# Performance work log

Hardware: AMD Instinct MI355X
Metric: run time of the kernel (lower is better)

## Reference

```python
import jax, jax.numpy as jnp
import numpy as np

E = 8          # num_experts
TOP_K = 2      # num_experts_per_tok
H = 1024       # hidden_size
F = 2048       # intermediate_size
B, S = 2, 4096


def setup_inputs() -> dict:
    key = jax.random.key(0)
    ks = jax.random.split(key, 5)
    hidden_states = jax.random.normal(ks[0], (B, S, H), dtype=jnp.float32)
    gate_w = jax.random.normal(ks[1], (E, H), dtype=jnp.float32) * 0.02   # router: logits = x @ gate_w.T
    Wg = jax.random.normal(ks[2], (E, H, F), dtype=jnp.float32) * 0.02    # gate_proj per expert
    Wu = jax.random.normal(ks[3], (E, H, F), dtype=jnp.float32) * 0.02    # up_proj per expert
    Wd = jax.random.normal(ks[4], (E, F, H), dtype=jnp.float32) * 0.02    # down_proj per expert
    return {"hidden_states": hidden_states, "gate_w": gate_w, "Wg": Wg, "Wu": Wu, "Wd": Wd}


def reference(hidden_states, gate_w, Wg, Wu, Wd):
    b, s, h = hidden_states.shape
    x = hidden_states.reshape(-1, h)                       # [T, H]
    T = x.shape[0]

    router_logits = x @ gate_w.T                           # [T, E]
    probs = jax.nn.softmax(router_logits.astype(jnp.float32), axis=-1)
    topk_w, topk_idx = jax.lax.top_k(probs, TOP_K)         # [T, K]
    topk_w = topk_w / jnp.sum(topk_w, axis=-1, keepdims=True)  # norm_topk_prob
    topk_w = topk_w.astype(x.dtype)

    # Dense per-token-per-expert combine weight (0 for unselected experts).
    w_full = jnp.zeros((T, E), dtype=x.dtype)
    w_full = w_full.at[jnp.arange(T)[:, None], topk_idx].add(topk_w)  # [T, E]

    out = jnp.zeros_like(x)
    for e in range(E):  # fixed small loop over experts
        g = jax.nn.silu(x @ Wg[e]) * (x @ Wu[e])           # [T, F]
        out = out + w_full[:, e:e + 1] * (g @ Wd[e])       # [T, H]

    return out.reshape(b, s, h), router_logits
```

## Files before the change

### kernel.cpp

```cpp
#include <hip/hip_runtime.h>
#include <cstdint>

#define NTOK   8192
#define HDIM   1024
#define FDIM   2048
#define NEXP   8
#define RTOT   (2*NTOK)
#define RPAD   128

typedef unsigned short u16;
typedef short   bf16x8 __attribute__((ext_vector_type(8)));
typedef float   f32x4  __attribute__((ext_vector_type(4)));
typedef u16     u16x8  __attribute__((ext_vector_type(8)));

__device__ __forceinline__ u16 f2bf(float v) {
  union { float f; uint32_t u; } a; a.f = v;
  uint32_t r = a.u + 0x7FFFu + ((a.u >> 16) & 1u);
  return (u16)(r >> 16);
}
__device__ __forceinline__ float bf2f(u16 b) {
  union { uint32_t u; float f; } a; a.u = ((uint32_t)b) << 16; return a.f;
}

__global__ void router_kernel(const float* __restrict__ x, const float* __restrict__ gw,
                              float* __restrict__ logits, int* __restrict__ te,
                              float* __restrict__ tw) {
  int gid  = blockIdx.x * blockDim.x + threadIdx.x;
  int t    = gid >> 6;
  int lane = gid & 63;
  const float4* xr = (const float4*)(x + (size_t)t * HDIM);
  float acc[NEXP];
#pragma unroll
  for (int e = 0; e < NEXP; ++e) acc[e] = 0.f;
#pragma unroll
  for (int c = 0; c < 4; ++c) {
    float4 xv = xr[c * 64 + lane];
#pragma unroll
    for (int e = 0; e < NEXP; ++e) {
      float4 wv = ((const float4*)(gw + e * HDIM))[c * 64 + lane];
      acc[e] += xv.x * wv.x + xv.y * wv.y + xv.z * wv.z + xv.w * wv.w;
    }
  }
#pragma unroll
  for (int off = 32; off > 0; off >>= 1)
#pragma unroll
    for (int e = 0; e < NEXP; ++e) acc[e] += __shfl_xor(acc[e], off, 64);

  if (lane == 0) {
#pragma unroll
    for (int e = 0; e < NEXP; ++e) logits[(size_t)t * NEXP + e] = acc[e];
    int e1 = 0;
#pragma unroll
    for (int e = 1; e < NEXP; ++e) if (acc[e] > acc[e1]) e1 = e;
    int e2 = -1;
#pragma unroll
    for (int e = 0; e < NEXP; ++e) {
      if (e == e1) continue;
      if (e2 < 0 || acc[e] > acc[e2]) e2 = e;
    }
    float m  = fmaxf(acc[e1], acc[e2]);
    float p1 = __expf(acc[e1] - m), p2 = __expf(acc[e2] - m);
    float inv = 1.f / (p1 + p2);
    te[t * 2]     = e1;  tw[t * 2]     = p1 * inv;
    te[t * 2 + 1] = e2;  tw[t * 2 + 1] = p2 * inv;
  }
}

__global__ void count_prefix_kernel(const int* __restrict__ te, int* __restrict__ offs,
                                    int* __restrict__ cursors) {
  __shared__ int wsum[16][NEXP];
  int cnt[NEXP];
#pragma unroll
  for (int e = 0; e < NEXP; ++e) cnt[e] = 0;
  for (int i = threadIdx.x; i < 2 * NTOK; i += 1024) {
    int v = te[i];
#pragma unroll
    for (int e = 0; e < NEXP; ++e) cnt[e] += (v == e) ? 1 : 0;
  }
#pragma unroll
  for (int off = 32; off > 0; off >>= 1)
#pragma unroll
    for (int e = 0; e < NEXP; ++e) cnt[e] += __shfl_xor(cnt[e], off, 64);
  int wave = threadIdx.x >> 6, lane = threadIdx.x & 63;
  if (lane == 0)
#pragma unroll
    for (int e = 0; e < NEXP; ++e) wsum[wave][e] = cnt[e];
  __syncthreads();
  if (threadIdx.x == 0) {
    int s = 0;
    for (int e = 0; e < NEXP; ++e) {
      int c = 0;
      for (int w = 0; w < 16; ++w) c += wsum[w][e];
      offs[e] = s; cursors[e * 16] = s; s += c;
    }
    offs[NEXP] = s;
  }
}

__global__ void scatter_kernel(const int* __restrict__ te, const float* __restrict__ tw,
                               int* __restrict__ cursors, int* __restrict__ tok_ids,
                               float* __restrict__ wts, int* __restrict__ slots) {
  int t    = blockIdx.x * blockDim.x + threadIdx.x;
  int lane = threadIdx.x & 63;
#pragma unroll
  for (int s = 0; s < 2; ++s) {
    int   e = te[t * 2 + s];
    float w = tw[t * 2 + s];
    int pos = 0;
#pragma unroll
    for (int e0 = 0; e0 < NEXP; ++e0) {
      unsigned long long m = __ballot(e == e0);
      if (e == e0) {
        int leader = __ffsll((unsigned long long)m) - 1;
        int rank   = __popcll(m & ((1ull << lane) - 1ull));
        int b = 0;
        if (lane == leader) b = atomicAdd(&cursors[e0 * 16], (int)__popcll(m));
        b = __shfl(b, leader, 64);
        pos = b + rank;
      }
    }
    tok_ids[pos] = t;
    wts[pos] = w;
    slots[t * 2 + s] = pos;
  }
}

__global__ void gather_cast_kernel(const float* __restrict__ x, const int* __restrict__ tok_ids,
                                   u16* __restrict__ Xg) {
  int j = blockIdx.x;
  int t = tok_ids[j];
  float4 v = ((const float4*)(x + (size_t)t * HDIM))[threadIdx.x];
  ushort4 o;
  o.x = f2bf(v.x); o.y = f2bf(v.y); o.z = f2bf(v.z); o.w = f2bf(v.w);
  ((ushort4*)(Xg + (size_t)j * HDIM))[threadIdx.x] = o;
}

__global__ __launch_bounds__(256)
void prep_weights_kernel(const float* __restrict__ Wg, const float* __restrict__ Wu,
                         const float* __restrict__ Wd, u16* __restrict__ Wgt,
                         u16* __restrict__ Wut, u16* __restrict__ Wdt) {
  __shared__ float tile[64 * 65];
  const int mat = blockIdx.z >> 3;
  const int e   = blockIdx.z & 7;
  const int K   = (mat < 2) ? HDIM : FDIM;
  const int N   = (mat < 2) ? FDIM : HDIM;
  const float* src = ((mat == 0) ? Wg : (mat == 1) ? Wu : Wd) + (size_t)e * K * N;
  u16*         dst = ((mat == 0) ? Wgt : (mat == 1) ? Wut : Wdt) + (size_t)e * K * N;
  const int tn = (mat < 2) ? blockIdx.x : blockIdx.y;
  const int tk = (mat < 2) ? blockIdx.y : blockIdx.x;
  const int k0 = tk * 64, n0 = tn * 64;

  const int r  = threadIdx.x >> 2;
  const int c4 = threadIdx.x & 3;
#pragma unroll
  for (int i = 0; i < 4; ++i) {
    int c = (c4 + i * 4) * 4;
    float4 v = *(const float4*)(src + (size_t)(k0 + r) * N + n0 + c);
    tile[r * 65 + c]     = v.x;
    tile[r * 65 + c + 1] = v.y;
    tile[r * 65 + c + 2] = v.z;
    tile[r * 65 + c + 3] = v.w;
  }
  __syncthreads();

  const int kq = threadIdx.x & 7;
  const int nr = threadIdx.x >> 3;
#pragma unroll
  for (int p = 0; p < 2; ++p) {
    int n = p * 32 + nr;
    u16x8 pk;
#pragma unroll
    for (int j = 0; j < 8; ++j)
      pk[j] = f2bf(tile[(kq * 8 + j) * 65 + n]);
    *(u16x8*)(dst + (size_t)(n0 + n) * K + k0 + kq * 8) = pk;
  }
}

__device__ __forceinline__ void stage_tile(const u16* __restrict__ src, int ld,
                                           u16* __restrict__ lds, int wave, int lane) {
#pragma unroll
  for (int i = 0; i < 4; ++i) {
    int chunk = ((i << 2) + wave) << 9;
    int flat  = chunk + (lane << 3);
    int row   = flat >> 6;
    int km    = (flat & 63) ^ ((row & 7) << 3);
    __builtin_amdgcn_global_load_lds(
        (const __attribute__((address_space(1))) uint32_t*)(src + (size_t)row * ld + km),
        (__attribute__((address_space(3))) uint32_t*)(lds + chunk),
        16, 0, 0);
  }
}

__global__ __launch_bounds__(256, 2)
void gemm1_kernel(const u16* __restrict__ Xg, const u16* __restrict__ Wgt,
                  const u16* __restrict__ Wut, const int* __restrict__ offs,
                  u16* __restrict__ G) {
  const int e     = blockIdx.z;
  const int rbase = offs[e];
  const int rows  = offs[e + 1] - rbase;
  const int row0  = blockIdx.y * 128;
  if (row0 >= rows) return;
  const int n0    = blockIdx.x * 128;
  const int arow0 = rbase + row0;

  __shared__ __align__(16) u16 As[128 * 64];
  __shared__ __align__(16) u16 Bgs[128 * 64];
  __shared__ __align__(16) u16 Bus[128 * 64];

  const int tid  = threadIdx.x;
  const int wave = tid >> 6;
  const int lane = tid & 63;
  const int wm   = wave >> 1, wn = wave & 1;
  const int l15  = lane & 15, quad = lane >> 4;

  const u16* Ag = Xg  + (size_t)arow0 * HDIM;
  const u16* Bg = Wgt + (size_t)e * FDIM * HDIM + (size_t)n0 * HDIM;
  const u16* Bu = Wut + (size_t)e * FDIM * HDIM + (size_t)n0 * HDIM;

  f32x4 accg[4][4], accu[4][4];
#pragma unroll
  for (int i = 0; i < 4; ++i)
#pragma unroll
    for (int j = 0; j < 4; ++j) { accg[i][j] = (f32x4)0.f; accu[i][j] = (f32x4)0.f; }

  for (int kt = 0; kt < HDIM / 64; ++kt) {
    const int k0 = kt * 64;
    stage_tile(Ag + k0, HDIM, As,  wave, lane);
    stage_tile(Bg + k0, HDIM, Bgs, wave, lane);
    stage_tile(Bu + k0, HDIM, Bus, wave, lane);
    __syncthreads();
#pragma unroll
    for (int kk = 0; kk < 64; kk += 32) {
      bf16x8 af[4];
#pragma unroll
      for (int im = 0; im < 4; ++im) {
        int r  = wm * 64 + im * 16 + l15;
        int kq = (kk + quad * 8) ^ ((r & 7) << 3);
        af[im] = *(const bf16x8*)(As + r * 64 + kq);
      }
#pragma unroll
      for (int in = 0; in < 4; ++in) {
        int r  = wn * 64 + in * 16 + l15;
        int kq = (kk + quad * 8) ^ ((r & 7) << 3);
        bf16x8 bg = *(const bf16x8*)(Bgs + r * 64 + kq);
        bf16x8 bu = *(const bf16x8*)(Bus + r * 64 + kq);
#pragma unroll
        for (int im = 0; im < 4; ++im) {
          accg[im][in] = __builtin_amdgcn_mfma_f32_16x16x32_bf16(af[im], bg, accg[im][in], 0, 0, 0);
          accu[im][in] = __builtin_amdgcn_mfma_f32_16x16x32_bf16(af[im], bu, accu[im][in], 0, 0, 0);
        }
      }
    }
    __syncthreads();
  }

#pragma unroll
  for (int im = 0; im < 4; ++im) {
#pragma unroll
    for (int rr = 0; rr < 4; ++rr) {
      int lrow = row0 + wm * 64 + im * 16 + quad * 4 + rr;
      if (lrow < rows) {
        size_t grow = (size_t)(rbase + lrow);
#pragma unroll
        for (int in = 0; in < 4; ++in) {
          float g = accg[im][in][rr];
          float u = accu[im][in][rr];
          float val = g / (1.f + __expf(-g)) * u;
          int gcol = n0 + wn * 64 + in * 16 + l15;
          G[grow * FDIM + gcol] = f2bf(val);
        }
      }
    }
  }
}

__global__ __launch_bounds__(256, 2)
void gemm2_kernel(const u16* __restrict__ G, const u16* __restrict__ Wdt,
                  const int* __restrict__ offs, const float* __restrict__ wts,
                  u16* __restrict__ Y) {
  const int e     = blockIdx.z;
  const int rbase = offs[e];
  const int rows  = offs[e + 1] - rbase;
  const int row0  = blockIdx.y * 128;
  if (row0 >= rows) return;
  const int n0    = blockIdx.x * 128;
  const int arow0 = rbase + row0;

  __shared__ __align__(16) u16 As[128 * 64];
  __shared__ __align__(16) u16 Bs[128 * 64];

  const int tid  = threadIdx.x;
  const int wave = tid >> 6;
  const int lane = tid & 63;
  const int wm   = wave >> 1, wn = wave & 1;
  const int l15  = lane & 15, quad = lane >> 4;

  const u16* Ag = G   + (size_t)arow0 * FDIM;
  const u16* Bg = Wdt + (size_t)e * HDIM * FDIM + (size_t)n0 * FDIM;

  f32x4 acc[4][4];
#pragma unroll
  for (int i = 0; i < 4; ++i)
#pragma unroll
    for (int j = 0; j < 4; ++j) acc[i][j] = (f32x4)0.f;

  for (int kt = 0; kt < FDIM / 64; ++kt) {
    const int k0 = kt * 64;
    stage_tile(Ag + k0, FDIM, As, wave, lane);
    stage_tile(Bg + k0, FDIM, Bs, wave, lane);
    __syncthreads();
#pragma unroll
    for (int kk = 0; kk < 64; kk += 32) {
      bf16x8 af[4], bf[4];
#pragma unroll
      for (int im = 0; im < 4; ++im) {
        int r  = wm * 64 + im * 16 + l15;
        int kq = (kk + quad * 8) ^ ((r & 7) << 3);
        af[im] = *(const bf16x8*)(As + r * 64 + kq);
      }
#pragma unroll
      for (int in = 0; in < 4; ++in) {
        int r  = wn * 64 + in * 16 + l15;
        int kq = (kk + quad * 8) ^ ((r & 7) << 3);
        bf[in] = *(const bf16x8*)(Bs + r * 64 + kq);
      }
#pragma unroll
      for (int in = 0; in < 4; ++in)
#pragma unroll
        for (int im = 0; im < 4; ++im)
          acc[im][in] = __builtin_amdgcn_mfma_f32_16x16x32_bf16(af[im], bf[in], acc[im][in], 0, 0, 0);
    }
    __syncthreads();
  }

#pragma unroll
  for (int im = 0; im < 4; ++im) {
#pragma unroll
    for (int rr = 0; rr < 4; ++rr) {
      int lrow = row0 + wm * 64 + im * 16 + quad * 4 + rr;
      if (lrow < rows) {
        int grow = rbase + lrow;
        float w  = wts[grow];
        u16* yrow = Y + (size_t)grow * HDIM + n0 + wn * 64 + l15;
#pragma unroll
        for (int in = 0; in < 4; ++in)
          yrow[in * 16] = f2bf(acc[im][in][rr] * w);
      }
    }
  }
}

__global__ void combine_kernel(const u16* __restrict__ Y, const int* __restrict__ slots,
                               float* __restrict__ out) {
  int t  = blockIdx.x;
  int s1 = slots[2 * t], s2 = slots[2 * t + 1];
  ushort4 a = ((const ushort4*)(Y + (size_t)s1 * HDIM))[threadIdx.x];
  ushort4 b = ((const ushort4*)(Y + (size_t)s2 * HDIM))[threadIdx.x];
  float4 o;
  o.x = bf2f(a.x) + bf2f(b.x);
  o.y = bf2f(a.y) + bf2f(b.y);
  o.z = bf2f(a.z) + bf2f(b.z);
  o.w = bf2f(a.w) + bf2f(b.w);
  ((float4*)(out + (size_t)t * HDIM))[threadIdx.x] = o;
}

extern "C" void kernel_launch(void* const* d_in, const int* in_sizes, int n_in,
                              void* d_out, int out_size, void* d_ws, size_t ws_size,
                              hipStream_t stream) {
  const float* x  = (const float*)d_in[0];
  const float* gw = (const float*)d_in[1];
  const float* Wg = (const float*)d_in[2];
  const float* Wu = (const float*)d_in[3];
  const float* Wd = (const float*)d_in[4];

  float* out    = (float*)d_out;
  float* logits = out + (size_t)NTOK * HDIM;

  char* p = (char*)d_ws;
  u16* Wgt = (u16*)p;  p += (size_t)NEXP * FDIM * HDIM * 2;
  u16* Wut = (u16*)p;  p += (size_t)NEXP * FDIM * HDIM * 2;
  u16* Wdt = (u16*)p;  p += (size_t)NEXP * HDIM * FDIM * 2;
  u16* Xg  = (u16*)p;  p += (size_t)(RTOT + RPAD) * HDIM * 2;
  u16* G   = (u16*)p;  p += (size_t)(RTOT + RPAD) * FDIM * 2;
  int*   tok_ids = (int*)p;   p += (RTOT + RPAD) * 4;
  float* wts     = (float*)p; p += (RTOT + RPAD) * 4;
  int*   te      = (int*)p;   p += NTOK * 2 * 4;
  float* tw      = (float*)p; p += NTOK * 2 * 4;
  int*   slots   = (int*)p;   p += NTOK * 2 * 4;
  int*   offs    = (int*)p;   p += (NEXP + 1) * 4;
  int*   cursors = (int*)p;   p += NEXP * 16 * 4;

  u16* Y = Xg;

  router_kernel<<<(NTOK * 64) / 256, 256, 0, stream>>>(x, gw, logits, te, tw);
  count_prefix_kernel<<<1, 1024, 0, stream>>>(te, offs, cursors);
  scatter_kernel<<<NTOK / 256, 256, 0, stream>>>(te, tw, cursors, tok_ids, wts, slots);
  gather_cast_kernel<<<RTOT, 256, 0, stream>>>(x, tok_ids, Xg);

  prep_weights_kernel<<<dim3(32, 16, 24), 256, 0, stream>>>(Wg, Wu, Wd, Wgt, Wut, Wdt);

  gemm1_kernel<<<dim3(FDIM / 128, 64, NEXP), 256, 0, stream>>>(Xg, Wgt, Wut, offs, G);
  gemm2_kernel<<<dim3(HDIM / 128, 64, NEXP), 256, 0, stream>>>(G, Wdt, offs, wts, Y);
  combine_kernel<<<NTOK, 256, 0, stream>>>(Y, slots, out);
}
```

Measured before the change: 554.9 us.

## Rewrite expert GEMMs as 256x128 tiles, 8 waves, double-buffered LDS pipeline

Both grouped GEMMs move from 128x128 tiles with 4 waves to 256x128 tiles with 8 waves. LDS is double-buffered, and the global-to-LDS loads for the next K-tile are interleaved with the MFMA phases. Explicit vmcnt waits, raw barriers, sched_barriers and setprio control the schedule. The aim is to hide load latency behind compute and raise operand reuse per block. In exchange, the larger LDS footprint (96KB for gemm1) may limit occupancy, the larger row tile wastes more work on padding, and the hand-placed waits and barriers are fragile.

```diff
diff --git a/kernel.cpp b/kernel.cpp
--- a/kernel.cpp
+++ b/kernel.cpp
@@ -6,7 +6,7 @@
 #define FDIM   2048
 #define NEXP   8
 #define RTOT   (2*NTOK)
-#define RPAD   128
+#define RPAD   256
 
 typedef unsigned short u16;
 typedef short   bf16x8 __attribute__((ext_vector_type(8)));
@@ -176,178 +176,273 @@
   }
 }
 
-__device__ __forceinline__ void stage_tile(const u16* __restrict__ src, int ld,
+
+#define BARRIER()  asm volatile("s_barrier" ::: "memory")
+#define SCHEDB()   __builtin_amdgcn_sched_barrier(0)
+#define WAITVM(n)  asm volatile("s_waitcnt vmcnt(" #n ")" ::: "memory")
+
+__device__ __forceinline__ void stage_half(const u16* __restrict__ src, int ld,
                                            u16* __restrict__ lds, int wave, int lane) {
 #pragma unroll
-  for (int i = 0; i < 4; ++i) {
-    int chunk = ((i << 2) + wave) << 9;
-    int flat  = chunk + (lane << 3);
-    int row   = flat >> 6;
-    int km    = (flat & 63) ^ ((row & 7) << 3);
+  for (int s = 0; s < 2; ++s) {
+    const int base = (s * 8 + wave) << 9;
+    const int flat = base + (lane << 3);
+    const int row  = flat >> 6;
+    const int km   = (flat & 63) ^ ((row & 7) << 3);
     __builtin_amdgcn_global_load_lds(
         (const __attribute__((address_space(1))) uint32_t*)(src + (size_t)row * ld + km),
-        (__attribute__((address_space(3))) uint32_t*)(lds + chunk),
+        (__attribute__((address_space(3))) uint32_t*)(lds + base),
         16, 0, 0);
   }
 }
 
-__global__ __launch_bounds__(256, 2)
+template<int MH>
+__device__ __forceinline__ void rd_a(const u16* __restrict__ buf, bf16x8 (&aH)[2][4],
+                                     int wm, int l15, int quad) {
+#pragma unroll
+  for (int k2 = 0; k2 < 2; ++k2)
+#pragma unroll
+    for (int im = 0; im < 4; ++im) {
+      const int r  = MH * 128 + wm * 64 + im * 16 + l15;
+      const int kq = (k2 * 32 + quad * 8) ^ ((r & 7) << 3);
+      aH[k2][im] = *(const bf16x8*)(buf + r * 64 + kq);
+    }
+}
+
+__device__ __forceinline__ void rd_b(const u16* __restrict__ buf, int rb, bf16x8 (&bb)[2][2],
+                                     int l15, int quad) {
+#pragma unroll
+  for (int k2 = 0; k2 < 2; ++k2)
+#pragma unroll
+    for (int in = 0; in < 2; ++in) {
+      const int r  = rb + in * 16 + l15;
+      const int kq = (k2 * 32 + quad * 8) ^ ((r & 7) << 3);
+      bb[k2][in] = *(const bf16x8*)(buf + r * 64 + kq);
+    }
+}
+
+__device__ __forceinline__ void mm16(const bf16x8 (&aH)[2][4], const bf16x8 (&bb)[2][2],
+                                     f32x4 (&ac)[4][2]) {
+#pragma unroll
+  for (int k2 = 0; k2 < 2; ++k2)
+#pragma unroll
+    for (int im = 0; im < 4; ++im)
+#pragma unroll
+      for (int in = 0; in < 2; ++in)
+        ac[im][in] = __builtin_amdgcn_mfma_f32_16x16x32_bf16(aH[k2][im], bb[k2][in],
+                                                             ac[im][in], 0, 0, 0);
+}
+
+__global__ __launch_bounds__(512, 2)
 void gemm1_kernel(const u16* __restrict__ Xg, const u16* __restrict__ Wgt,
                   const u16* __restrict__ Wut, const int* __restrict__ offs,
                   u16* __restrict__ G) {
   const int e     = blockIdx.z;
   const int rbase = offs[e];
   const int rows  = offs[e + 1] - rbase;
-  const int row0  = blockIdx.y * 128;
+  const int row0  = blockIdx.y * 256;
   if (row0 >= rows) return;
   const int n0    = blockIdx.x * 128;
-  const int arow0 = rbase + row0;
-
-  __shared__ __align__(16) u16 As[128 * 64];
-  __shared__ __align__(16) u16 Bgs[128 * 64];
-  __shared__ __align__(16) u16 Bus[128 * 64];
+
+  __shared__ __align__(16) u16 As [2][256 * 64];
+  __shared__ __align__(16) u16 Bgs[2][128 * 64];
+  __shared__ __align__(16) u16 Bus[2][128 * 64];
 
   const int tid  = threadIdx.x;
   const int wave = tid >> 6;
   const int lane = tid & 63;
-  const int wm   = wave >> 1, wn = wave & 1;
+  const int wm   = wave >> 2, wn = wave & 3;
   const int l15  = lane & 15, quad = lane >> 4;
 
-  const u16* Ag = Xg  + (size_t)arow0 * HDIM;
-  const u16* Bg = Wgt + (size_t)e * FDIM * HDIM + (size_t)n0 * HDIM;
-  const u16* Bu = Wut + (size_t)e * FDIM * HDIM + (size_t)n0 * HDIM;
-
-  f32x4 accg[4][4], accu[4][4];
-#pragma unroll
-  for (int i = 0; i < 4; ++i)
-#pragma unroll
-    for (int j = 0; j < 4; ++j) { accg[i][j] = (f32x4)0.f; accu[i][j] = (f32x4)0.f; }
-
-  for (int kt = 0; kt < HDIM / 64; ++kt) {
-    const int k0 = kt * 64;
-    stage_tile(Ag + k0, HDIM, As,  wave, lane);
-    stage_tile(Bg + k0, HDIM, Bgs, wave, lane);
-    stage_tile(Bu + k0, HDIM, Bus, wave, lane);
-    __syncthreads();
-#pragma unroll
-    for (int kk = 0; kk < 64; kk += 32) {
-      bf16x8 af[4];
-#pragma unroll
-      for (int im = 0; im < 4; ++im) {
-        int r  = wm * 64 + im * 16 + l15;
-        int kq = (kk + quad * 8) ^ ((r & 7) << 3);
-        af[im] = *(const bf16x8*)(As + r * 64 + kq);
-      }
-#pragma unroll
-      for (int in = 0; in < 4; ++in) {
-        int r  = wn * 64 + in * 16 + l15;
-        int kq = (kk + quad * 8) ^ ((r & 7) << 3);
-        bf16x8 bg = *(const bf16x8*)(Bgs + r * 64 + kq);
-        bf16x8 bu = *(const bf16x8*)(Bus + r * 64 + kq);
-#pragma unroll
-        for (int im = 0; im < 4; ++im) {
-          accg[im][in] = __builtin_amdgcn_mfma_f32_16x16x32_bf16(af[im], bg, accg[im][in], 0, 0, 0);
-          accu[im][in] = __builtin_amdgcn_mfma_f32_16x16x32_bf16(af[im], bu, accu[im][in], 0, 0, 0);
+  const u16* Ap  = Xg  + (size_t)(rbase + row0) * HDIM;
+  const u16* Bgp = Wgt + (size_t)e * FDIM * HDIM + (size_t)n0 * HDIM;
+  const u16* Bup = Wut + (size_t)e * FDIM * HDIM + (size_t)n0 * HDIM;
+
+  f32x4 accg[2][4][2], accu[2][4][2];
+#pragma unroll
+  for (int h = 0; h < 2; ++h)
+#pragma unroll
+    for (int i = 0; i < 4; ++i)
+#pragma unroll
+      for (int j = 0; j < 2; ++j) { accg[h][i][j] = (f32x4)0.f; accu[h][i][j] = (f32x4)0.f; }
+
+  bf16x8 aH[2][4], bg[2][2], bu[2][2];
+
+  stage_half(Ap,                         HDIM, As[0],            wave, lane); SCHEDB();
+  stage_half(Bgp,                        HDIM, Bgs[0],           wave, lane); SCHEDB();
+  stage_half(Bup,                        HDIM, Bus[0],           wave, lane); SCHEDB();
+  stage_half(Ap + (size_t)128 * HDIM,    HDIM, As[0] + 128 * 64, wave, lane);
+  WAITVM(4); BARRIER(); SCHEDB();
+
+  const int NT = HDIM / 64;
+  int b = 0;
+  for (int kt = 0; kt < NT - 1; ++kt) {
+    const u16* An  = Ap  + 64;
+    const u16* Bgn = Bgp + 64;
+    const u16* Bun = Bup + 64;
+    const u16* Ac  = As[b];  const u16* Bgc = Bgs[b]; const u16* Buc = Bus[b];
+    u16* Ax = As[b ^ 1]; u16* Bgx = Bgs[b ^ 1]; u16* Bux = Bus[b ^ 1];
+
+    rd_a<0>(Ac, aH, wm, l15, quad);
+    rd_b(Bgc, wn * 32, bg, l15, quad);
+    stage_half(An, HDIM, Ax, wave, lane);
+    WAITVM(4); BARRIER(); SCHEDB();
+    __builtin_amdgcn_s_setprio(1);
+    mm16(aH, bg, accg[0]);
+    __builtin_amdgcn_s_setprio(0);
+    BARRIER(); SCHEDB();
+
+    rd_b(Buc, wn * 32, bu, l15, quad);
+    stage_half(Bgn, HDIM, Bgx, wave, lane);
+    WAITVM(4); BARRIER(); SCHEDB();
+    __builtin_amdgcn_s_setprio(1);
+    mm16(aH, bu, accu[0]);
+    __builtin_amdgcn_s_setprio(0);
+    BARRIER(); SCHEDB();
+
+    rd_a<1>(Ac, aH, wm, l15, quad);
+    stage_half(Bun, HDIM, Bux, wave, lane);
+    BARRIER(); SCHEDB();
+    __builtin_amdgcn_s_setprio(1);
+    mm16(aH, bg, accg[1]);
+    __builtin_amdgcn_s_setprio(0);
+    BARRIER(); SCHEDB();
+
+    stage_half(An + (size_t)128 * HDIM, HDIM, Ax + 128 * 64, wave, lane);
+    WAITVM(4); BARRIER(); SCHEDB();
+    __builtin_amdgcn_s_setprio(1);
+    mm16(aH, bu, accu[1]);
+    __builtin_amdgcn_s_setprio(0);
+    BARRIER(); SCHEDB();
+
+    Ap = An; Bgp = Bgn; Bup = Bun; b ^= 1;
+  }
+  {
+    const u16* Ac = As[b]; const u16* Bgc = Bgs[b]; const u16* Buc = Bus[b];
+    rd_a<0>(Ac, aH, wm, l15, quad);
+    rd_b(Bgc, wn * 32, bg, l15, quad);
+    WAITVM(2); BARRIER(); SCHEDB();
+    mm16(aH, bg, accg[0]);
+    rd_b(Buc, wn * 32, bu, l15, quad);
+    mm16(aH, bu, accu[0]);
+    WAITVM(0); BARRIER(); SCHEDB();
+    rd_a<1>(Ac, aH, wm, l15, quad);
+    mm16(aH, bg, accg[1]);
+    mm16(aH, bu, accu[1]);
+  }
+
+#pragma unroll
+  for (int mh = 0; mh < 2; ++mh)
+#pragma unroll
+    for (int im = 0; im < 4; ++im)
+#pragma unroll
+      for (int rr = 0; rr < 4; ++rr) {
+        int lrow = row0 + mh * 128 + wm * 64 + im * 16 + quad * 4 + rr;
+        if (lrow < rows) {
+          size_t grow = (size_t)(rbase + lrow);
+#pragma unroll
+          for (int in = 0; in < 2; ++in) {
+            float g = accg[mh][im][in][rr];
+            float u = accu[mh][im][in][rr];
+            float val = g / (1.f + __expf(-g)) * u;
+            G[grow * FDIM + n0 + wn * 32 + in * 16 + l15] = f2bf(val);
+          }
         }
       }
-    }
-    __syncthreads();
-  }
-
-#pragma unroll
-  for (int im = 0; im < 4; ++im) {
-#pragma unroll
-    for (int rr = 0; rr < 4; ++rr) {
-      int lrow = row0 + wm * 64 + im * 16 + quad * 4 + rr;
-      if (lrow < rows) {
-        size_t grow = (size_t)(rbase + lrow);
-#pragma unroll
-        for (int in = 0; in < 4; ++in) {
-          float g = accg[im][in][rr];
-          float u = accu[im][in][rr];
-          float val = g / (1.f + __expf(-g)) * u;
-          int gcol = n0 + wn * 64 + in * 16 + l15;
-          G[grow * FDIM + gcol] = f2bf(val);
-        }
-      }
-    }
-  }
-}
-
-__global__ __launch_bounds__(256, 2)
+}
+
+__global__ __launch_bounds__(512, 2)
 void gemm2_kernel(const u16* __restrict__ G, const u16* __restrict__ Wdt,
                   const int* __restrict__ offs, const float* __restrict__ wts,
                   u16* __restrict__ Y) {
   const int e     = blockIdx.z;
   const int rbase = offs[e];
   const int rows  = offs[e + 1] - rbase;
-  const int row0  = blockIdx.y * 128;
+  const int row0  = blockIdx.y * 256;
   if (row0 >= rows) return;
   const int n0    = blockIdx.x * 128;
-  const int arow0 = rbase + row0;
-
-  __shared__ __align__(16) u16 As[128 * 64];
-  __shared__ __align__(16) u16 Bs[128 * 64];
+
+  __shared__ __align__(16) u16 As[2][256 * 64];
+  __shared__ __align__(16) u16 Bs[2][128 * 64];
 
   const int tid  = threadIdx.x;
   const int wave = tid >> 6;
   const int lane = tid & 63;
-  const int wm   = wave >> 1, wn = wave & 1;
+  const int wm   = wave >> 2, wn = wave & 3;
   const int l15  = lane & 15, quad = lane >> 4;
 
-  const u16* Ag = G   + (size_t)arow0 * FDIM;
-  const u16* Bg = Wdt + (size_t)e * HDIM * FDIM + (size_t)n0 * FDIM;
-
-  f32x4 acc[4][4];
-#pragma unroll
-  for (int i = 0; i < 4; ++i)
-#pragma unroll
-    for (int j = 0; j < 4; ++j) acc[i][j] = (f32x4)0.f;
-
-  for (int kt = 0; kt < FDIM / 64; ++kt) {
-    const int k0 = kt * 64;
-    stage_tile(Ag + k0, FDIM, As, wave, lane);
-    stage_tile(Bg + k0, FDIM, Bs, wave, lane);
-    __syncthreads();
-#pragma unroll
-    for (int kk = 0; kk < 64; kk += 32) {
-      bf16x8 af[4], bf[4];
-#pragma unroll
-      for (int im = 0; im < 4; ++im) {
-        int r  = wm * 64 + im * 16 + l15;
-        int kq = (kk + quad * 8) ^ ((r & 7) << 3);
-        af[im] = *(const bf16x8*)(As + r * 64 + kq);
+  const u16* Ap = G   + (size_t)(rbase + row0) * FDIM;
+  const u16* Bp = Wdt + (size_t)e * HDIM * FDIM + (size_t)n0 * FDIM;
+
+  f32x4 acc[2][4][2];
+#pragma unroll
+  for (int h = 0; h < 2; ++h)
+#pragma unroll
+    for (int i = 0; i < 4; ++i)
+#pragma unroll
+      for (int j = 0; j < 2; ++j) acc[h][i][j] = (f32x4)0.f;
+
+  bf16x8 aH[2][4], bb[2][2];
+
+  stage_half(Ap,                      FDIM, As[0],            wave, lane); SCHEDB();
+  stage_half(Bp,                      FDIM, Bs[0],            wave, lane); SCHEDB();
+  stage_half(Ap + (size_t)128 * FDIM, FDIM, As[0] + 128 * 64, wave, lane);
+  WAITVM(2); BARRIER(); SCHEDB();
+
+  const int NT = FDIM / 64;
+  int b = 0;
+  for (int kt = 0; kt < NT - 1; ++kt) {
+    const u16* An = Ap + 64;
+    const u16* Bn = Bp + 64;
+    const u16* Ac = As[b]; const u16* Bc = Bs[b];
+    u16* Ax = As[b ^ 1]; u16* Bx = Bs[b ^ 1];
+
+    rd_a<0>(Ac, aH, wm, l15, quad);
+    rd_b(Bc, wn * 32, bb, l15, quad);
+    stage_half(An, FDIM, Ax, wave, lane); SCHEDB();
+    stage_half(Bn, FDIM, Bx, wave, lane);
+    WAITVM(4); BARRIER(); SCHEDB();
+    __builtin_amdgcn_s_setprio(1);
+    mm16(aH, bb, acc[0]);
+    __builtin_amdgcn_s_setprio(0);
+    BARRIER(); SCHEDB();
+
+    rd_a<1>(Ac, aH, wm, l15, quad);
+    stage_half(An + (size_t)128 * FDIM, FDIM, Ax + 128 * 64, wave, lane);
+    WAITVM(2); BARRIER(); SCHEDB();
+    __builtin_amdgcn_s_setprio(1);
+    mm16(aH, bb, acc[1]);
+    __builtin_amdgcn_s_setprio(0);
+    BARRIER(); SCHEDB();
+
+    Ap = An; Bp = Bn; b ^= 1;
+  }
+  {
+    const u16* Ac = As[b]; const u16* Bc = Bs[b];
+    rd_a<0>(Ac, aH, wm, l15, quad);
+    rd_b(Bc, wn * 32, bb, l15, quad);
+    mm16(aH, bb, acc[0]);
+    WAITVM(0); BARRIER(); SCHEDB();
+    rd_a<1>(Ac, aH, wm, l15, quad);
+    mm16(aH, bb, acc[1]);
+  }
+
+#pragma unroll
+  for (int mh = 0; mh < 2; ++mh)
+#pragma unroll
+    for (int im = 0; im < 4; ++im)
+#pragma unroll
+      for (int rr = 0; rr < 4; ++rr) {
+        int lrow = row0 + mh * 128 + wm * 64 + im * 16 + quad * 4 + rr;
+        if (lrow < rows) {
+          int grow = rbase + lrow;
+          float w  = wts[grow];
+          u16* yrow = Y + (size_t)grow * HDIM + n0 + wn * 32 + l15;
+#pragma unroll
+          for (int in = 0; in < 2; ++in)
+            yrow[in * 16] = f2bf(acc[mh][im][in][rr] * w);
+        }
       }
-#pragma unroll
-      for (int in = 0; in < 4; ++in) {
-        int r  = wn * 64 + in * 16 + l15;
-        int kq = (kk + quad * 8) ^ ((r & 7) << 3);
-        bf[in] = *(const bf16x8*)(Bs + r * 64 + kq);
-      }
-#pragma unroll
-      for (int in = 0; in < 4; ++in)
-#pragma unroll
-        for (int im = 0; im < 4; ++im)
-          acc[im][in] = __builtin_amdgcn_mfma_f32_16x16x32_bf16(af[im], bf[in], acc[im][in], 0, 0, 0);
-    }
-    __syncthreads();
-  }
-
-#pragma unroll
-  for (int im = 0; im < 4; ++im) {
-#pragma unroll
-    for (int rr = 0; rr < 4; ++rr) {
-      int lrow = row0 + wm * 64 + im * 16 + quad * 4 + rr;
-      if (lrow < rows) {
-        int grow = rbase + lrow;
-        float w  = wts[grow];
-        u16* yrow = Y + (size_t)grow * HDIM + n0 + wn * 64 + l15;
-#pragma unroll
-        for (int in = 0; in < 4; ++in)
-          yrow[in * 16] = f2bf(acc[im][in][rr] * w);
-      }
-    }
-  }
 }
 
 __global__ void combine_kernel(const u16* __restrict__ Y, const int* __restrict__ slots,
@@ -399,7 +494,7 @@
 
   prep_weights_kernel<<<dim3(32, 16, 24), 256, 0, stream>>>(Wg, Wu, Wd, Wgt, Wut, Wdt);
 
-  gemm1_kernel<<<dim3(FDIM / 128, 64, NEXP), 256, 0, stream>>>(Xg, Wgt, Wut, offs, G);
-  gemm2_kernel<<<dim3(HDIM / 128, 64, NEXP), 256, 0, stream>>>(G, Wdt, offs, wts, Y);
+  gemm1_kernel<<<dim3(FDIM / 128, 64, NEXP), 512, 0, stream>>>(Xg, Wgt, Wut, offs, G);
+  gemm2_kernel<<<dim3(HDIM / 128, 64, NEXP), 512, 0, stream>>>(G, Wdt, offs, wts, Y);
   combine_kernel<<<NTOK, 256, 0, stream>>>(Y, slots, out);
 }
```

Measured after the change: 579.0 us. 4.3% more time.

## Fuse MoE combine into gemm2 epilogue via atomic adds into output

Applied to the files above, without the earlier changes.

The down-projection GEMM now scatters its weighted results straight into the fp32 output with atomicAdd, indexed through tok_ids. This removes the bf16 Y intermediate, the slots array and the separate combine kernel. A memset of the output is added up front. In exchange, each output element takes two scattered atomic fp32 adds that are not coalesced, the summation order becomes nondeterministic, and the memset is extra traffic.

```diff
diff --git a/kernel.cpp b/kernel.cpp
--- a/kernel.cpp
+++ b/kernel.cpp
@@ -99,7 +99,7 @@
 
 __global__ void scatter_kernel(const int* __restrict__ te, const float* __restrict__ tw,
                                int* __restrict__ cursors, int* __restrict__ tok_ids,
-                               float* __restrict__ wts, int* __restrict__ slots) {
+                               float* __restrict__ wts) {
   int t    = blockIdx.x * blockDim.x + threadIdx.x;
   int lane = threadIdx.x & 63;
 #pragma unroll
@@ -121,7 +121,6 @@
     }
     tok_ids[pos] = t;
     wts[pos] = w;
-    slots[t * 2 + s] = pos;
   }
 }
 
@@ -277,7 +276,7 @@
 __global__ __launch_bounds__(256, 2)
 void gemm2_kernel(const u16* __restrict__ G, const u16* __restrict__ Wdt,
                   const int* __restrict__ offs, const float* __restrict__ wts,
-                  u16* __restrict__ Y) {
+                  const int* __restrict__ tok_ids, float* __restrict__ out) {
   const int e     = blockIdx.z;
   const int rbase = offs[e];
   const int rows  = offs[e + 1] - rbase;
@@ -341,27 +340,14 @@
       if (lrow < rows) {
         int grow = rbase + lrow;
         float w  = wts[grow];
-        u16* yrow = Y + (size_t)grow * HDIM + n0 + wn * 64 + l15;
+        int   t  = tok_ids[grow];
+        float* orow = out + (size_t)t * HDIM + n0 + wn * 64 + l15;
 #pragma unroll
         for (int in = 0; in < 4; ++in)
-          yrow[in * 16] = f2bf(acc[im][in][rr] * w);
-      }
-    }
-  }
-}
-
-__global__ void combine_kernel(const u16* __restrict__ Y, const int* __restrict__ slots,
-                               float* __restrict__ out) {
-  int t  = blockIdx.x;
-  int s1 = slots[2 * t], s2 = slots[2 * t + 1];
-  ushort4 a = ((const ushort4*)(Y + (size_t)s1 * HDIM))[threadIdx.x];
-  ushort4 b = ((const ushort4*)(Y + (size_t)s2 * HDIM))[threadIdx.x];
-  float4 o;
-  o.x = bf2f(a.x) + bf2f(b.x);
-  o.y = bf2f(a.y) + bf2f(b.y);
-  o.z = bf2f(a.z) + bf2f(b.z);
-  o.w = bf2f(a.w) + bf2f(b.w);
-  ((float4*)(out + (size_t)t * HDIM))[threadIdx.x] = o;
+          atomicAdd(orow + in * 16, acc[im][in][rr] * w);
+      }
+    }
+  }
 }
 
 extern "C" void kernel_launch(void* const* d_in, const int* in_sizes, int n_in,
@@ -386,20 +372,18 @@
   float* wts     = (float*)p; p += (RTOT + RPAD) * 4;
   int*   te      = (int*)p;   p += NTOK * 2 * 4;
   float* tw      = (float*)p; p += NTOK * 2 * 4;
-  int*   slots   = (int*)p;   p += NTOK * 2 * 4;
   int*   offs    = (int*)p;   p += (NEXP + 1) * 4;
   int*   cursors = (int*)p;   p += NEXP * 16 * 4;
 
-  u16* Y = Xg;
+  hipMemsetAsync(out, 0, (size_t)NTOK * HDIM * sizeof(float), stream);
 
   router_kernel<<<(NTOK * 64) / 256, 256, 0, stream>>>(x, gw, logits, te, tw);
   count_prefix_kernel<<<1, 1024, 0, stream>>>(te, offs, cursors);
-  scatter_kernel<<<NTOK / 256, 256, 0, stream>>>(te, tw, cursors, tok_ids, wts, slots);
+  scatter_kernel<<<NTOK / 256, 256, 0, stream>>>(te, tw, cursors, tok_ids, wts);
   gather_cast_kernel<<<RTOT, 256, 0, stream>>>(x, tok_ids, Xg);
 
   prep_weights_kernel<<<dim3(32, 16, 24), 256, 0, stream>>>(Wg, Wu, Wd, Wgt, Wut, Wdt);
 
   gemm1_kernel<<<dim3(FDIM / 128, 64, NEXP), 256, 0, stream>>>(Xg, Wgt, Wut, offs, G);
-  gemm2_kernel<<<dim3(HDIM / 128, 64, NEXP), 256, 0, stream>>>(G, Wdt, offs, wts, Y);
-  combine_kernel<<<NTOK, 256, 0, stream>>>(Y, slots, out);
-}
+  gemm2_kernel<<<dim3(HDIM / 128, 64, NEXP), 256, 0, stream>>>(G, Wdt, offs, wts, tok_ids, out);
+}
```

Result: slower. 569.6 us (+2.6%).
